# Optimization experiments

Hardware: AMD Instinct MI355X
Metric: run time of the kernel (lower is better)

Reference implementation:

```python
import jax, jax.numpy as jnp
import numpy as np

B, S, F = 4, 2048, 8
D, H, L, FF = 256, 8, 2, 1024
DH = D // H
NSK, NPAT = 2000, 64
DQ = D // 4  # pattern/feat sub-embedding width


def setup_inputs() -> dict:
    key = jax.random.key(0)
    ks = jax.random.split(key, 32)
    r = lambda i, shape: jax.random.normal(ks[i], shape, jnp.float32) * 0.02
    return {
        'interactions': jax.random.randint(ks[0], (B, S), 0, 2 * NSK),
        'patterns': jax.random.randint(ks[1], (B, S), 0, NPAT),
        'forget_features': jax.random.normal(ks[2], (B, S, F), jnp.float32),
        'inter_emb': r(3, (2 * NSK, D)),
        'pattern_emb': r(4, (NPAT, DQ)),
        'feat_W': r(5, (F, DQ)), 'feat_b': jnp.zeros((DQ,), jnp.float32),
        'in_W': r(6, (D + 2 * DQ, D)), 'in_b': jnp.zeros((D,), jnp.float32),
        'time_W': r(7, (1, D)), 'time_b': jnp.zeros((D,), jnp.float32),
        'pos_W': r(8, (1, D)), 'pos_b': jnp.zeros((D,), jnp.float32),
        'Wq': r(9, (L, D, H, DH)), 'bq': jnp.zeros((L, H, DH), jnp.float32),
        'Wk': r(10, (L, D, H, DH)), 'bk': jnp.zeros((L, H, DH), jnp.float32),
        'Wv': r(11, (L, D, H, DH)), 'bv': jnp.zeros((L, H, DH), jnp.float32),
        'Wo': r(12, (L, H, DH, D)), 'bo': jnp.zeros((L, D), jnp.float32),
        'kerple_p': jnp.full((L, H, 1, 1), 0.5, jnp.float32),
        'kerple_a': jnp.zeros((L, H, 1, 1), jnp.float32),
        'ln1_g': jnp.ones((L, D), jnp.float32), 'ln1_b': jnp.zeros((L, D), jnp.float32),
        'ln2_g': jnp.ones((L, D), jnp.float32), 'ln2_b': jnp.zeros((L, D), jnp.float32),
        'ffn_W1': r(13, (L, D, FF)), 'ffn_b1': jnp.zeros((L, FF), jnp.float32),
        'ffn_W2': r(14, (L, FF, D)), 'ffn_b2': jnp.zeros((L, D), jnp.float32),
        'out_W': r(15, (D, NSK)), 'out_b': jnp.zeros((NSK,), jnp.float32),
    }


def _ln(x, g, b, eps=1e-6):
    m = jnp.mean(x, -1, keepdims=True)
    v = jnp.mean(jnp.square(x - m), -1, keepdims=True)
    return g * (x - m) * jax.lax.rsqrt(v + eps) + b


def reference(interactions, patterns, forget_features, inter_emb, pattern_emb,
              feat_W, feat_b, in_W, in_b, time_W, time_b, pos_W, pos_b,
              Wq, bq, Wk, bk, Wv, bv, Wo, bo, kerple_p, kerple_a,
              ln1_g, ln1_b, ln2_g, ln2_b, ffn_W1, ffn_b1, ffn_W2, ffn_b2,
              out_W, out_b):
    inter_e = inter_emb[interactions]                      # [B,S,D]
    pat_e = pattern_emb[patterns]                          # [B,S,D/4]
    feat_e = forget_features @ feat_W + feat_b             # [B,S,D/4]
    x = jnp.concatenate([inter_e, pat_e, feat_e], -1) @ in_W + in_b  # [B,S,D]
    elapsed = forget_features[:, :, 0:1]
    time_enc = jnp.tanh(elapsed @ time_W + time_b)
    pos = jnp.arange(S, dtype=jnp.float32)[None, :, None] / jnp.float32(S)
    pos_enc = pos @ pos_W + pos_b
    x = x + time_enc + pos_enc

    positions = jnp.arange(S, dtype=jnp.float32)
    dist = jnp.maximum(positions[:, None] - positions[None, :], 0.0)  # [S,S]
    causal_bias = jnp.triu(jnp.full((S, S), -1e9, jnp.float32), 1)    # [S,S]
    inv_sqrt_dh = 1.0 / jnp.sqrt(jnp.float32(DH))

    for i in range(L):
        p = jax.nn.softplus(kerple_p[i])                   # [H,1,1]
        a = jax.nn.softplus(kerple_a[i])
        bias = causal_bias[None] - p * jnp.log1p(a * dist[None])  # [H,S,S]
        q = jnp.einsum('bsd,dhk->bshk', x, Wq[i]) + bq[i]
        k = jnp.einsum('bsd,dhk->bshk', x, Wk[i]) + bk[i]
        v = jnp.einsum('bsd,dhk->bshk', x, Wv[i]) + bv[i]
        scores = jnp.einsum('bshk,bthk->bhst', q, k) * inv_sqrt_dh + bias[None]
        attn = jax.nn.softmax(scores, axis=-1)
        o = jnp.einsum('bhst,bthk->bshk', attn, v)
        attn_out = jnp.einsum('bshk,hkd->bsd', o, Wo[i]) + bo[i]
        x = _ln(x + attn_out, ln1_g[i], ln1_b[i])
        h = jax.nn.gelu(x @ ffn_W1[i] + ffn_b1[i], approximate=False)
        ffn_out = h @ ffn_W2[i] + ffn_b2[i]
        x = _ln(x + ffn_out, ln2_g[i], ln2_b[i])
    return x @ out_W + out_b
```

## Files before the change

### kernel.cpp

```cpp
#include <hip/hip_runtime.h>
#include <math.h>

#define SEQ   2048
#define BATCH 4
#define NTOK  8192
#define DM    256
#define NHD   8
#define DHD   32
#define DFF   1024
#define NSKC  2000

typedef __attribute__((ext_vector_type(8))) short short8;
typedef __attribute__((ext_vector_type(4))) float f32x4;
typedef unsigned short ushort_t;

#define QPRE ((float)(0.17677669529663687 * 1.4426950408889634))

#define SPERM(i) (((i) & ~31) | (((i) & 15) << 1) | (((i) >> 4) & 1))

__device__ __forceinline__ ushort_t f2bf(float x) {
    union { float f; unsigned u; } c; c.f = x;
    unsigned r = c.u + 0x7FFFu + ((c.u >> 16) & 1u);
    return (ushort_t)(r >> 16);
}

#if __has_builtin(__builtin_amdgcn_cvt_pk_bf16_f32)
typedef __attribute__((ext_vector_type(2))) __bf16 bf16x2_t;
__device__ __forceinline__ unsigned pack_bf16(float a, float b) {
    bf16x2_t r = __builtin_amdgcn_cvt_pk_bf16_f32(a, b);
    union { bf16x2_t v; unsigned u; } c; c.v = r;
    return c.u;
}
#else
__device__ __forceinline__ unsigned pack_bf16(float a, float b) {
    return (unsigned)f2bf(a) | ((unsigned)f2bf(b) << 16);
}
#endif

__device__ __forceinline__ float bf2f(ushort_t x) {
    union { unsigned u; float f; } c; c.u = ((unsigned)x) << 16;
    return c.f;
}

struct ConvSeg { const float* src; ushort_t* dst; int K; int N; int ntx; int base; int kperm; };
struct ConvArgs { ConvSeg s[14]; };

__global__ __launch_bounds__(256) void convert_kernel(ConvArgs args) {
    int bid = blockIdx.x;
    int si = 0;
#pragma unroll
    for (int i = 1; i < 14; i++) if (bid >= args.s[i].base) si = i;
    ConvSeg sg = args.s[si];
    int local = bid - sg.base;
    int ty = local / sg.ntx;
    int tx = local - ty * sg.ntx;
    int n0 = tx * 32, k0 = ty * 32;
    __shared__ float T[32][33];
    int tid = threadIdx.x;
    int tn = tid & 31, tk4 = tid >> 5;
#pragma unroll
    for (int i = 0; i < 4; i++) {
        int kl = tk4 + i * 8;
        float v = 0.0f;
        if (n0 + tn < sg.N) v = sg.src[(size_t)(k0 + kl) * sg.N + n0 + tn];
        T[kl][tn] = v;
    }
    __syncthreads();
    int tk = tid & 31, tn4 = tid >> 5;
    int tks = sg.kperm ? (((tk & 15) << 1) | ((tk >> 4) & 1)) : tk;
#pragma unroll
    for (int i = 0; i < 4; i++) {
        int nl = tn4 + i * 8;
        sg.dst[(size_t)(n0 + nl) * sg.K + k0 + tks] = f2bf(T[tk][nl]);
    }
}

__global__ __launch_bounds__(384) void concat_kernel(
    const int* __restrict__ interactions, const int* __restrict__ patterns,
    const float* __restrict__ ff, const float* __restrict__ inter_emb,
    const float* __restrict__ pattern_emb, const float* __restrict__ feat_W,
    const float* __restrict__ feat_b, ushort_t* __restrict__ out)
{
    int tok = blockIdx.x;
    int j = threadIdx.x;
    float v;
    if (j < 256) {
        v = inter_emb[(size_t)interactions[tok] * 256 + j];
    } else if (j < 320) {
        v = pattern_emb[patterns[tok] * 64 + (j - 256)];
    } else {
        int c = j - 320;
        float acc = feat_b[c];
#pragma unroll
        for (int f = 0; f < 8; f++) acc += ff[tok * 8 + f] * feat_W[f * 64 + c];
        v = acc;
    }
    out[(size_t)tok * 384 + j] = f2bf(v);
}

__global__ __launch_bounds__(256) void ln_kernel(
    float* __restrict__ x, const ushort_t* __restrict__ r,
    const float* __restrict__ g, const float* __restrict__ b,
    ushort_t* __restrict__ xb)
{
    int tok = blockIdx.x;
    int d = threadIdx.x;
    int ds = SPERM(d);
    size_t row = (size_t)tok * DM;
    float v = x[row + d] + bf2f(r[row + ds]);
    float s1 = v, s2 = v * v;
#pragma unroll
    for (int off = 32; off > 0; off >>= 1) {
        s1 += __shfl_down(s1, off, 64);
        s2 += __shfl_down(s2, off, 64);
    }
    __shared__ float red1[4], red2[4];
    int wid = d >> 6, lane = d & 63;
    if (lane == 0) { red1[wid] = s1; red2[wid] = s2; }
    __syncthreads();
    s1 = red1[0] + red1[1] + red1[2] + red1[3];
    s2 = red2[0] + red2[1] + red2[2] + red2[3];
    float mean = s1 * (1.0f / 256.0f);
    float var = s2 * (1.0f / 256.0f) - mean * mean;
    float inv = rsqrtf(var + 1e-6f);
    float nv = g[d] * (v - mean) * inv + b[d];
    x[row + d] = nv;
    xb[row + ds] = f2bf(nv);
}

__global__ __launch_bounds__(256) void gemm64(
    const ushort_t* __restrict__ A, const ushort_t* __restrict__ Bt,
    int M, int N, int K, int mode,
    float* __restrict__ Cf, ushort_t* __restrict__ Cb,
    const float* __restrict__ b0,
    const float* __restrict__ ffg, const float* __restrict__ tW,
    const float* __restrict__ tb, const float* __restrict__ pW,
    const float* __restrict__ pb)
{
    __shared__ ushort_t As[2][64][40];
    __shared__ ushort_t Bs[2][64][40];
    int m0 = blockIdx.x * 64, n0 = blockIdx.y * 64;
    int tid = threadIdx.x;
    int wv = tid >> 6, lane = tid & 63;
    int quad = lane >> 4, l16 = lane & 15;
    int srow = tid >> 2, sc = (tid & 3) << 3;

    f32x4 acc[4];
#pragma unroll
    for (int j = 0; j < 4; j++) acc[j] = (f32x4){0.f, 0.f, 0.f, 0.f};

    uint4 pa = *(const uint4*)&A[(size_t)(m0 + srow) * K + sc];
    uint4 pbv = *(const uint4*)&Bt[(size_t)(n0 + srow) * K + sc];
    *(uint4*)&As[0][srow][sc] = pa;
    *(uint4*)&Bs[0][srow][sc] = pbv;

    int mrow = wv * 16;
    for (int k0 = 0; k0 < K; k0 += 32) {
        int cur = (k0 >> 5) & 1;
        __syncthreads();
        bool more = (k0 + 32 < K);
        if (more) {
            pa = *(const uint4*)&A[(size_t)(m0 + srow) * K + k0 + 32 + sc];
            pbv = *(const uint4*)&Bt[(size_t)(n0 + srow) * K + k0 + 32 + sc];
        }
        short8 af = *(const short8*)&As[cur][mrow + l16][quad * 8];
        short8 bf0 = *(const short8*)&Bs[cur][l16][quad * 8];
        short8 bf1 = *(const short8*)&Bs[cur][16 + l16][quad * 8];
        short8 bf2 = *(const short8*)&Bs[cur][32 + l16][quad * 8];
        short8 bf3 = *(const short8*)&Bs[cur][48 + l16][quad * 8];
        acc[0] = __builtin_amdgcn_mfma_f32_16x16x32_bf16(af, bf0, acc[0], 0, 0, 0);
        acc[1] = __builtin_amdgcn_mfma_f32_16x16x32_bf16(af, bf1, acc[1], 0, 0, 0);
        acc[2] = __builtin_amdgcn_mfma_f32_16x16x32_bf16(af, bf2, acc[2], 0, 0, 0);
        acc[3] = __builtin_amdgcn_mfma_f32_16x16x32_bf16(af, bf3, acc[3], 0, 0, 0);
        if (more) {
            *(uint4*)&As[cur ^ 1][srow][sc] = pa;
            *(uint4*)&Bs[cur ^ 1][srow][sc] = pbv;
        }
    }

#pragma unroll
    for (int r = 0; r < 4; r++) {
        int m = m0 + mrow + quad * 4 + r;
        if (mode == 4) {
            int s = m & (SEQ - 1);
            float el = ffg[m * 8];
            float pos = (float)s * (1.0f / (float)SEQ);
#pragma unroll
            for (int nt = 0; nt < 4; nt += 2) {
                int nlo = n0 + nt * 16 + l16;
                int nhi = nlo + 16;
                float v0 = acc[nt][r] + b0[nlo] + tanhf(el * tW[nlo] + tb[nlo]) + pos * pW[nlo] + pb[nlo];
                float v1 = acc[nt + 1][r] + b0[nhi] + tanhf(el * tW[nhi] + tb[nhi]) + pos * pW[nhi] + pb[nhi];
                Cf[(size_t)m * N + nlo] = v0;
                Cf[(size_t)m * N + nhi] = v1;
                *(unsigned*)&Cb[(size_t)m * N + n0 + nt * 16 + 2 * l16] = pack_bf16(v0, v1);
            }
        } else {
#pragma unroll
            for (int nt = 0; nt < 4; nt += 2) {
                int nlo = n0 + nt * 16 + l16;
                float v0 = acc[nt][r] + b0[nlo];
                float v1 = acc[nt + 1][r] + b0[nlo + 16];
                *(unsigned*)&Cb[(size_t)m * N + n0 + nt * 16 + 2 * l16] = pack_bf16(v0, v1);
            }
        }
    }
}

__global__ __launch_bounds__(256) void gemm_db(
    const ushort_t* __restrict__ A, const ushort_t* __restrict__ Bt,
    int M, int N, int K, int mode,
    ushort_t* __restrict__ Cb, ushort_t* __restrict__ Ck, ushort_t* __restrict__ Cv,
    const float* __restrict__ b0, const float* __restrict__ b1,
    const float* __restrict__ b2)
{
    __shared__ ushort_t As[2][128][40];
    __shared__ ushort_t Bs[2][64][40];
    int m0 = blockIdx.x * 128, n0 = blockIdx.y * 64;
    int tid = threadIdx.x;
    int wv = tid >> 6, lane = tid & 63;
    int quad = lane >> 4, l16 = lane & 15;
    int srow = tid >> 2, sc = (tid & 3) << 3;

    f32x4 acc[2][4];
#pragma unroll
    for (int i = 0; i < 2; i++)
#pragma unroll
        for (int j = 0; j < 4; j++) acc[i][j] = (f32x4){0.f, 0.f, 0.f, 0.f};

    uint4 pa0 = *(const uint4*)&A[(size_t)(m0 + srow) * K + sc];
    uint4 pa1 = *(const uint4*)&A[(size_t)(m0 + 64 + srow) * K + sc];
    uint4 pbb = *(const uint4*)&Bt[(size_t)(n0 + srow) * K + sc];
    *(uint4*)&As[0][srow][sc] = pa0;
    *(uint4*)&As[0][64 + srow][sc] = pa1;
    *(uint4*)&Bs[0][srow][sc] = pbb;

    int msub = wv * 32;
    for (int k0 = 0; k0 < K; k0 += 32) {
        int cur = (k0 >> 5) & 1;
        __syncthreads();
        bool more = (k0 + 32 < K);
        if (more) {
            pa0 = *(const uint4*)&A[(size_t)(m0 + srow) * K + k0 + 32 + sc];
            pa1 = *(const uint4*)&A[(size_t)(m0 + 64 + srow) * K + k0 + 32 + sc];
            pbb = *(const uint4*)&Bt[(size_t)(n0 + srow) * K + k0 + 32 + sc];
        }
        short8 af0 = *(const short8*)&As[cur][msub + l16][quad * 8];
        short8 af1 = *(const short8*)&As[cur][msub + 16 + l16][quad * 8];
        short8 bf0 = *(const short8*)&Bs[cur][l16][quad * 8];
        short8 bf1 = *(const short8*)&Bs[cur][16 + l16][quad * 8];
        short8 bf2 = *(const short8*)&Bs[cur][32 + l16][quad * 8];
        short8 bf3 = *(const short8*)&Bs[cur][48 + l16][quad * 8];
        acc[0][0] = __builtin_amdgcn_mfma_f32_16x16x32_bf16(af0, bf0, acc[0][0], 0, 0, 0);
        acc[0][1] = __builtin_amdgcn_mfma_f32_16x16x32_bf16(af0, bf1, acc[0][1], 0, 0, 0);
        acc[0][2] = __builtin_amdgcn_mfma_f32_16x16x32_bf16(af0, bf2, acc[0][2], 0, 0, 0);
        acc[0][3] = __builtin_amdgcn_mfma_f32_16x16x32_bf16(af0, bf3, acc[0][3], 0, 0, 0);
        acc[1][0] = __builtin_amdgcn_mfma_f32_16x16x32_bf16(af1, bf0, acc[1][0], 0, 0, 0);
        acc[1][1] = __builtin_amdgcn_mfma_f32_16x16x32_bf16(af1, bf1, acc[1][1], 0, 0, 0);
        acc[1][2] = __builtin_amdgcn_mfma_f32_16x16x32_bf16(af1, bf2, acc[1][2], 0, 0, 0);
        acc[1][3] = __builtin_amdgcn_mfma_f32_16x16x32_bf16(af1, bf3, acc[1][3], 0, 0, 0);
        if (more) {
            *(uint4*)&As[cur ^ 1][srow][sc] = pa0;
            *(uint4*)&As[cur ^ 1][64 + srow][sc] = pa1;
            *(uint4*)&Bs[cur ^ 1][srow][sc] = pbb;
        }
    }

#pragma unroll
    for (int mt = 0; mt < 2; mt++) {
#pragma unroll
        for (int nt = 0; nt < 4; nt += 2) {
            int nlo = n0 + nt * 16 + l16;
#pragma unroll
            for (int r = 0; r < 4; r++) {
                int m = m0 + msub + mt * 16 + quad * 4 + r;
                float vlo = acc[mt][nt][r];
                float vhi = acc[mt][nt + 1][r];
                if (mode == 1) {
                    float t0 = vlo + b0[nlo];
                    float t1 = vhi + b0[nlo + 16];
                    t0 = 0.5f * t0 * (1.0f + erff(t0 * 0.70710678118654752f));
                    t1 = 0.5f * t1 * (1.0f + erff(t1 * 0.70710678118654752f));
                    *(unsigned*)&Cb[(size_t)m * N + n0 + nt * 16 + 2 * l16] = pack_bf16(t0, t1);
                } else {
                    int which = nlo >> 8, idx = nlo & 255;
                    int hh = idx >> 5;
                    int s = m & (SEQ - 1), b = m >> 11;
                    if (which == 0) {
                        float q0 = (vlo + b0[idx]) * QPRE;
                        float q1 = (vhi + b0[idx + 16]) * QPRE;
                        *(unsigned*)&Cb[(((size_t)(b * NHD + hh)) * SEQ + s) * DHD + 2 * l16] = pack_bf16(q0, q1);
                    } else if (which == 1) {
                        float k0v = vlo + b1[idx];
                        float k1v = vhi + b1[idx + 16];
                        *(unsigned*)&Ck[(((size_t)(b * NHD + hh)) * SEQ + s) * DHD + 2 * l16] = pack_bf16(k0v, k1v);
                    } else {
                        int sp = (s & ~31) | (((s & 15) << 1) | ((s >> 4) & 1));
                        Cv[(((size_t)(b * NHD + hh)) * DHD + l16) * SEQ + sp] = f2bf(vlo + b2[idx]);
                        Cv[(((size_t)(b * NHD + hh)) * DHD + l16 + 16) * SEQ + sp] = f2bf(vhi + b2[idx + 16]);
                    }
                }
            }
        }
    }
}

__global__ __launch_bounds__(256) void gemm_out(
    const ushort_t* __restrict__ A, const ushort_t* __restrict__ Bt,
    int M, int N, int K,
    float* __restrict__ Cf, const float* __restrict__ b0, int Nreal)
{
    __shared__ ushort_t As[2][128][40];
    __shared__ ushort_t Bs[2][128][40];
    int m0 = blockIdx.x * 128, n0 = blockIdx.y * 128;
    int tid = threadIdx.x;
    int wv = tid >> 6, lane = tid & 63;
    int quad = lane >> 4, l16 = lane & 15;
    int wm = (wv >> 1) * 64, wn = (wv & 1) * 64;
    int srow = tid >> 1, sc = (tid & 1) << 4;

    f32x4 acc[4][4];
#pragma unroll
    for (int i = 0; i < 4; i++)
#pragma unroll
        for (int j = 0; j < 4; j++) acc[i][j] = (f32x4){0.f, 0.f, 0.f, 0.f};

    uint4 pa0 = *(const uint4*)&A[(size_t)(m0 + srow) * K + sc];
    uint4 pa1 = *(const uint4*)&A[(size_t)(m0 + srow) * K + sc + 8];
    uint4 pb0 = *(const uint4*)&Bt[(size_t)(n0 + srow) * K + sc];
    uint4 pb1 = *(const uint4*)&Bt[(size_t)(n0 + srow) * K + sc + 8];
    *(uint4*)&As[0][srow][sc] = pa0;
    *(uint4*)&As[0][srow][sc + 8] = pa1;
    *(uint4*)&Bs[0][srow][sc] = pb0;
    *(uint4*)&Bs[0][srow][sc + 8] = pb1;

    for (int k0 = 0; k0 < K; k0 += 32) {
        int cur = (k0 >> 5) & 1;
        __syncthreads();
        bool more = (k0 + 32 < K);
        if (more) {
            pa0 = *(const uint4*)&A[(size_t)(m0 + srow) * K + k0 + 32 + sc];
            pa1 = *(const uint4*)&A[(size_t)(m0 + srow) * K + k0 + 32 + sc + 8];
            pb0 = *(const uint4*)&Bt[(size_t)(n0 + srow) * K + k0 + 32 + sc];
            pb1 = *(const uint4*)&Bt[(size_t)(n0 + srow) * K + k0 + 32 + sc + 8];
        }
        short8 af[4], bf[4];
#pragma unroll
        for (int i = 0; i < 4; i++) {
            af[i] = *(const short8*)&As[cur][wm + i * 16 + l16][quad * 8];
            bf[i] = *(const short8*)&Bs[cur][wn + i * 16 + l16][quad * 8];
        }
#pragma unroll
        for (int i = 0; i < 4; i++)
#pragma unroll
            for (int j = 0; j < 4; j++)
                acc[i][j] = __builtin_amdgcn_mfma_f32_16x16x32_bf16(af[i], bf[j], acc[i][j], 0, 0, 0);
        if (more) {
            *(uint4*)&As[cur ^ 1][srow][sc] = pa0;
            *(uint4*)&As[cur ^ 1][srow][sc + 8] = pa1;
            *(uint4*)&Bs[cur ^ 1][srow][sc] = pb0;
            *(uint4*)&Bs[cur ^ 1][srow][sc + 8] = pb1;
        }
    }

#pragma unroll
    for (int i = 0; i < 4; i++) {
#pragma unroll
        for (int j = 0; j < 4; j++) {
            int n = n0 + wn + j * 16 + l16;
            if (n < Nreal) {
#pragma unroll
                for (int r = 0; r < 4; r++) {
                    int m = m0 + wm + i * 16 + quad * 4 + r;
                    Cf[(size_t)m * Nreal + n] = acc[i][j][r] + b0[n];
                }
            }
        }
    }
}

__global__ __launch_bounds__(256) void attn_mfma(
    const ushort_t* __restrict__ qb, const ushort_t* __restrict__ kb,
    const ushort_t* __restrict__ vtb, const float* __restrict__ kp,
    const float* __restrict__ ka, ushort_t* __restrict__ ob)
{
    int h = blockIdx.y, b = blockIdx.z;
    int tid = threadIdx.x, wv = tid >> 6, lane = tid & 63;
    int quad = lane >> 4, l16 = lane & 15;
    int pair = wv >> 1, parity = wv & 1;

    __shared__ float tabs[2112];
    __shared__ ushort_t P2[4][2][16 * 40];
    __shared__ float Cmb[2][64][28];

    float p = log1pf(__expf(kp[h]));
    float a = log1pf(__expf(ka[h]));
    for (int i = tid; i < 2112; i += 256) {
        float w = 0.0f;
        if (i >= 64) w = exp2f(-p * __log2f(fmaf(a, (float)(i - 64), 1.0f)));
        tabs[i] = w;
    }
    __syncthreads();

    int bh = b * NHD + h;
    const ushort_t* Qh = qb + (size_t)bh * SEQ * DHD;
    const ushort_t* Kh = kb + (size_t)bh * SEQ * DHD;
    const ushort_t* Vh = vtb + (size_t)bh * DHD * SEQ;

    int pj = blockIdx.x * 2 + pair;
    int tlo = pj, thi = 127 - pj;
    int qlo0 = tlo * 16, qhi0 = thi * 16;

    short8 qfl = *(const short8*)&Qh[(qlo0 + l16) * DHD + quad * 8];
    short8 qfh = *(const short8*)&Qh[(qhi0 + l16) * DHD + quad * 8];
    f32x4 ol0 = (f32x4){0.f,0.f,0.f,0.f}, ol1 = (f32x4){0.f,0.f,0.f,0.f};
    f32x4 oh0 = (f32x4){0.f,0.f,0.f,0.f}, oh1 = (f32x4){0.f,0.f,0.f,0.f};
    float lsl[4] = {0.f,0.f,0.f,0.f}, lsh[4] = {0.f,0.f,0.f,0.f};
    ushort_t* Pl = &P2[wv][0][0];
    ushort_t* Ph = &P2[wv][1][0];

    int nch_hi = (thi + 2) >> 1;
    int nch_lo = (tlo + 2) >> 1;
    int qsrh = qhi0 + quad * 4;
    int qsrl = qlo0 + quad * 4;

    for (int ch = parity; ch < nch_hi; ch += 2) {
        int k0 = ch * 32;
        short8 kf0 = *(const short8*)&Kh[(k0 + l16) * DHD + quad * 8];
        short8 kf1 = *(const short8*)&Kh[(k0 + 16 + l16) * DHD + quad * 8];
        short8 vf0 = *(const short8*)&Vh[l16 * SEQ + k0 + quad * 8];
        short8 vf1 = *(const short8*)&Vh[(16 + l16) * SEQ + k0 + quad * 8];
        f32x4 z = (f32x4){0.f,0.f,0.f,0.f};

        f32x4 s0 = __builtin_amdgcn_mfma_f32_16x16x32_bf16(qfh, kf0, z, 0, 0, 0);
        f32x4 s1 = __builtin_amdgcn_mfma_f32_16x16x32_bf16(qfh, kf1, z, 0, 0, 0);
        {
            const float* tp = &tabs[qsrh - k0 - l16 + 48];
#pragma unroll
            for (int r = 0; r < 4; r++) {
                float e0 = exp2f(s0[r]) * tp[16 + r];
                float e1 = exp2f(s1[r]) * tp[r];
                lsh[r] += e0 + e1;
                *(unsigned*)&Ph[(quad * 4 + r) * 40 + l16 * 2] = pack_bf16(e0, e1);
            }
        }
        bool do_lo = (ch < nch_lo);
        if (do_lo) {
            f32x4 t0 = __builtin_amdgcn_mfma_f32_16x16x32_bf16(qfl, kf0, z, 0, 0, 0);
            f32x4 t1 = __builtin_amdgcn_mfma_f32_16x16x32_bf16(qfl, kf1, z, 0, 0, 0);
            const float* tq = &tabs[qsrl - k0 - l16 + 48];
#pragma unroll
            for (int r = 0; r < 4; r++) {
                float e0 = exp2f(t0[r]) * tq[16 + r];
                float e1 = exp2f(t1[r]) * tq[r];
                lsl[r] += e0 + e1;
                *(unsigned*)&Pl[(quad * 4 + r) * 40 + l16 * 2] = pack_bf16(e0, e1);
            }
        }

        __builtin_amdgcn_wave_barrier();
        short8 pfh = *(const short8*)&Ph[l16 * 40 + quad * 8];
        oh0 = __builtin_amdgcn_mfma_f32_16x16x32_bf16(pfh, vf0, oh0, 0, 0, 0);
        oh1 = __builtin_amdgcn_mfma_f32_16x16x32_bf16(pfh, vf1, oh1, 0, 0, 0);
        if (do_lo) {
            short8 pfl = *(const short8*)&Pl[l16 * 40 + quad * 8];
            ol0 = __builtin_amdgcn_mfma_f32_16x16x32_bf16(pfl, vf0, ol0, 0, 0, 0);
            ol1 = __builtin_amdgcn_mfma_f32_16x16x32_bf16(pfl, vf1, ol1, 0, 0, 0);
        }
    }

    if (parity == 1) {
        float* cp = &Cmb[pair][lane][0];
        *(float4*)&cp[0]  = (float4){oh0[0], oh0[1], oh0[2], oh0[3]};
        *(float4*)&cp[4]  = (float4){oh1[0], oh1[1], oh1[2], oh1[3]};
        *(float4*)&cp[8]  = (float4){ol0[0], ol0[1], ol0[2], ol0[3]};
        *(float4*)&cp[12] = (float4){ol1[0], ol1[1], ol1[2], ol1[3]};
        *(float4*)&cp[16] = (float4){lsh[0], lsh[1], lsh[2], lsh[3]};
        *(float4*)&cp[20] = (float4){lsl[0], lsl[1], lsl[2], lsl[3]};
    }
    __syncthreads();
    if (parity == 0) {
        const float* cp = &Cmb[pair][lane][0];
#pragma unroll
        for (int i = 0; i < 4; i++) {
            oh0[i] += cp[i];      oh1[i] += cp[4 + i];
            ol0[i] += cp[8 + i];  ol1[i] += cp[12 + i];
            lsh[i] += cp[16 + i]; lsl[i] += cp[20 + i];
        }
#pragma unroll
        for (int r = 0; r < 4; r++) {
#pragma unroll
            for (int off = 1; off < 16; off <<= 1) {
                lsh[r] += __shfl_xor(lsh[r], off, 16);
                lsl[r] += __shfl_xor(lsl[r], off, 16);
            }
        }
#pragma unroll
        for (int r = 0; r < 4; r++) {
            float rh = 1.0f / lsh[r];
            float rl = 1.0f / lsl[r];
            size_t bh_ = ((size_t)(b * SEQ + qsrh + r)) * DM + h * DHD;
            size_t bl_ = ((size_t)(b * SEQ + qsrl + r)) * DM + h * DHD;
            *(unsigned*)&ob[bh_ + 2 * l16] = pack_bf16(oh0[r] * rh, oh1[r] * rh);
            *(unsigned*)&ob[bl_ + 2 * l16] = pack_bf16(ol0[r] * rl, ol1[r] * rl);
        }
    }
}

extern "C" void kernel_launch(void* const* d_in, const int* in_sizes, int n_in,
                              void* d_out, int out_size, void* d_ws, size_t ws_size,
                              hipStream_t stream) {
    const int*   interactions = (const int*)d_in[0];
    const int*   patterns     = (const int*)d_in[1];
    const float* ff           = (const float*)d_in[2];
    const float* inter_emb    = (const float*)d_in[3];
    const float* pattern_emb  = (const float*)d_in[4];
    const float* feat_W       = (const float*)d_in[5];
    const float* feat_b       = (const float*)d_in[6];
    const float* in_W         = (const float*)d_in[7];
    const float* in_b         = (const float*)d_in[8];
    const float* time_W       = (const float*)d_in[9];
    const float* time_b       = (const float*)d_in[10];
    const float* pos_W        = (const float*)d_in[11];
    const float* pos_b        = (const float*)d_in[12];
    const float* Wq           = (const float*)d_in[13];
    const float* bq           = (const float*)d_in[14];
    const float* Wk           = (const float*)d_in[15];
    const float* bk           = (const float*)d_in[16];
    const float* Wv           = (const float*)d_in[17];
    const float* bv           = (const float*)d_in[18];
    const float* Wo           = (const float*)d_in[19];
    const float* bo           = (const float*)d_in[20];
    const float* kerple_p     = (const float*)d_in[21];
    const float* kerple_a     = (const float*)d_in[22];
    const float* ln1_g        = (const float*)d_in[23];
    const float* ln1_b        = (const float*)d_in[24];
    const float* ln2_g        = (const float*)d_in[25];
    const float* ln2_b        = (const float*)d_in[26];
    const float* ffn_W1       = (const float*)d_in[27];
    const float* ffn_b1       = (const float*)d_in[28];
    const float* ffn_W2       = (const float*)d_in[29];
    const float* ffn_b2       = (const float*)d_in[30];
    const float* out_W        = (const float*)d_in[31];
    const float* out_b        = (const float*)d_in[32];
    float* out = (float*)d_out;

    char* wsb = (char*)d_ws;
    const size_t MB = 1024 * 1024;
    float*    x    = (float*)(wsb + 0);
    ushort_t* tmpb = (ushort_t*)(wsb + 8  * MB);
    ushort_t* xb   = (ushort_t*)(wsb + 16 * MB);
    ushort_t* qbuf = (ushort_t*)(wsb + 20 * MB);
    ushort_t* kbuf = (ushort_t*)(wsb + 24 * MB);
    ushort_t* vtbf = (ushort_t*)(wsb + 28 * MB);
    ushort_t* shrd = (ushort_t*)(wsb + 32 * MB);
    ushort_t* cbuf = shrd;
    ushort_t* o_bf = shrd;
    ushort_t* h_bf = shrd;
    char* wp = wsb + 48 * MB;
    ushort_t* inWt  = (ushort_t*)wp;  wp += 256  * 384 * 2;
    ushort_t* qkvWt = (ushort_t*)wp;  wp += 2 * 768 * 256 * 2;
    ushort_t* WoT   = (ushort_t*)wp;  wp += 2 * 256 * 256 * 2;
    ushort_t* W1T   = (ushort_t*)wp;  wp += 2 * 1024 * 256 * 2;
    ushort_t* W2T   = (ushort_t*)wp;  wp += 2 * 256 * 1024 * 2;
    ushort_t* outWt = (ushort_t*)wp;  wp += 2048 * 256 * 2;

    ConvArgs ca;
    int D2 = 256 * 256;
    int base = 0, ib = 0;
    auto addseg = [&](const float* src, ushort_t* dst, int K, int N, int Npad, int kp) {
        ca.s[ib].src = src; ca.s[ib].dst = dst; ca.s[ib].K = K; ca.s[ib].N = N;
        ca.s[ib].ntx = Npad / 32; ca.s[ib].base = base; ca.s[ib].kperm = kp;
        base += (Npad / 32) * (K / 32); ib++;
    };
    addseg(in_W,            inWt,           384,  256,  256,  0);
    addseg(Wq,              qkvWt,          256,  256,  256,  1);
    addseg(Wk,              qkvWt + 1 * D2, 256,  256,  256,  1);
    addseg(Wv,              qkvWt + 2 * D2, 256,  256,  256,  1);
    addseg(Wq + D2,         qkvWt + 3 * D2, 256,  256,  256,  1);
    addseg(Wk + D2,         qkvWt + 4 * D2, 256,  256,  256,  1);
    addseg(Wv + D2,         qkvWt + 5 * D2, 256,  256,  256,  1);
    addseg(Wo,              WoT,            256,  256,  256,  1);
    addseg(Wo + D2,         WoT + D2,       256,  256,  256,  1);
    addseg(ffn_W1,          W1T,            256,  1024, 1024, 1);
    addseg(ffn_W1 + 4 * D2, W1T + 4 * D2,   256,  1024, 1024, 1);
    addseg(ffn_W2,          W2T,            1024, 256,  256,  1);
    addseg(ffn_W2 + 4 * D2, W2T + 4 * D2,   1024, 256,  256,  1);
    addseg(out_W,           outWt,          256,  2000, 2048, 1);
    convert_kernel<<<base, 256, 0, stream>>>(ca);

    concat_kernel<<<NTOK, 384, 0, stream>>>(interactions, patterns, ff,
                                            inter_emb, pattern_emb, feat_W, feat_b, cbuf);
    gemm64<<<dim3(128, 4), 256, 0, stream>>>(cbuf, inWt, NTOK, 256, 384, 4,
                                             x, xb, in_b, ff, time_W, time_b, pos_W, pos_b);

    for (int l = 0; l < 2; l++) {
        gemm_db<<<dim3(64, 12), 256, 0, stream>>>(
            xb, qkvWt + (size_t)l * 768 * 256, NTOK, 768, 256, 2,
            qbuf, kbuf, vtbf, bq + l * 256, bk + l * 256, bv + l * 256);
        attn_mfma<<<dim3(32, NHD, BATCH), 256, 0, stream>>>(
            qbuf, kbuf, vtbf, kerple_p + l * NHD, kerple_a + l * NHD, o_bf);
        gemm64<<<dim3(128, 4), 256, 0, stream>>>(
            o_bf, WoT + (size_t)l * D2, NTOK, 256, 256, 5,
            nullptr, tmpb, bo + l * 256, nullptr, nullptr, nullptr, nullptr, nullptr);
        ln_kernel<<<NTOK, 256, 0, stream>>>(x, tmpb, ln1_g + l * 256, ln1_b + l * 256, xb);
        gemm_db<<<dim3(64, 16), 256, 0, stream>>>(
            xb, W1T + (size_t)l * 4 * D2, NTOK, 1024, 256, 1,
            h_bf, nullptr, nullptr, ffn_b1 + l * 1024, nullptr, nullptr);
        gemm64<<<dim3(128, 4), 256, 0, stream>>>(
            h_bf, W2T + (size_t)l * 4 * D2, NTOK, 256, 1024, 5,
            nullptr, tmpb, ffn_b2 + l * 256, nullptr, nullptr, nullptr, nullptr, nullptr);
        ln_kernel<<<NTOK, 256, 0, stream>>>(x, tmpb, ln2_g + l * 256, ln2_b + l * 256, xb);
    }

    gemm_out<<<dim3(64, 16), 256, 0, stream>>>(
        xb, outWt, NTOK, 2048, 256, out, out_b, NSKC);
}
```

Baseline: 418.5 us.

## Split attention key chunks across four waves per query-tile pair with K prefetch

Each attention block now handles one lo/hi query-tile pair, and its four waves stride over key chunks by four instead of two waves per pair striding by two. The grid doubles to 64 blocks in x. Partial outputs and row sums are combined through a two-stage shared-memory tree reduction, and the P scratch buffer is aliased onto the combine buffer to cut LDS use. Next-iteration K fragments are prefetched into registers to hide load latency. The cost is extra __syncthreads and reduction work per block, plus possible load imbalance for short low tiles.

```diff
diff --git a/kernel.cpp b/kernel.cpp
--- a/kernel.cpp
+++ b/kernel.cpp
@@ -387,11 +387,10 @@
     int h = blockIdx.y, b = blockIdx.z;
     int tid = threadIdx.x, wv = tid >> 6, lane = tid & 63;
     int quad = lane >> 4, l16 = lane & 15;
-    int pair = wv >> 1, parity = wv & 1;
 
     __shared__ float tabs[2112];
-    __shared__ ushort_t P2[4][2][16 * 40];
-    __shared__ float Cmb[2][64][28];
+    __shared__ __align__(16) float Cmbf[2][64][28];
+    ushort_t* P2 = (ushort_t*)&Cmbf[0][0][0];
 
     float p = log1pf(__expf(kp[h]));
     float a = log1pf(__expf(ka[h]));
@@ -407,7 +406,7 @@
     const ushort_t* Kh = kb + (size_t)bh * SEQ * DHD;
     const ushort_t* Vh = vtb + (size_t)bh * DHD * SEQ;
 
-    int pj = blockIdx.x * 2 + pair;
+    int pj = blockIdx.x;
     int tlo = pj, thi = 127 - pj;
     int qlo0 = tlo * 16, qhi0 = thi * 16;
 
@@ -416,20 +415,33 @@
     f32x4 ol0 = (f32x4){0.f,0.f,0.f,0.f}, ol1 = (f32x4){0.f,0.f,0.f,0.f};
     f32x4 oh0 = (f32x4){0.f,0.f,0.f,0.f}, oh1 = (f32x4){0.f,0.f,0.f,0.f};
     float lsl[4] = {0.f,0.f,0.f,0.f}, lsh[4] = {0.f,0.f,0.f,0.f};
-    ushort_t* Pl = &P2[wv][0][0];
-    ushort_t* Ph = &P2[wv][1][0];
+    ushort_t* Pl = P2 + wv * 1280;
+    ushort_t* Ph = Pl + 640;
 
     int nch_hi = (thi + 2) >> 1;
     int nch_lo = (tlo + 2) >> 1;
     int qsrh = qhi0 + quad * 4;
     int qsrl = qlo0 + quad * 4;
 
-    for (int ch = parity; ch < nch_hi; ch += 2) {
+    int ch = wv;
+    short8 kf0n, kf1n;
+    {
         int k0 = ch * 32;
-        short8 kf0 = *(const short8*)&Kh[(k0 + l16) * DHD + quad * 8];
-        short8 kf1 = *(const short8*)&Kh[(k0 + 16 + l16) * DHD + quad * 8];
+        kf0n = *(const short8*)&Kh[(k0 + l16) * DHD + quad * 8];
+        kf1n = *(const short8*)&Kh[(k0 + 16 + l16) * DHD + quad * 8];
+    }
+
+    for (; ch < nch_hi; ch += 4) {
+        int k0 = ch * 32;
+        short8 kf0 = kf0n, kf1 = kf1n;
         short8 vf0 = *(const short8*)&Vh[l16 * SEQ + k0 + quad * 8];
         short8 vf1 = *(const short8*)&Vh[(16 + l16) * SEQ + k0 + quad * 8];
+        int chn = ch + 4;
+        if (chn < nch_hi) {
+            int kn = chn * 32;
+            kf0n = *(const short8*)&Kh[(kn + l16) * DHD + quad * 8];
+            kf1n = *(const short8*)&Kh[(kn + 16 + l16) * DHD + quad * 8];
+        }
         f32x4 z = (f32x4){0.f,0.f,0.f,0.f};
 
         f32x4 s0 = __builtin_amdgcn_mfma_f32_16x16x32_bf16(qfh, kf0, z, 0, 0, 0);
@@ -469,8 +481,9 @@
         }
     }
 
-    if (parity == 1) {
-        float* cp = &Cmb[pair][lane][0];
+    __syncthreads();
+    float* cp = &Cmbf[wv >> 1][lane][0];
+    if (wv & 1) {
         *(float4*)&cp[0]  = (float4){oh0[0], oh0[1], oh0[2], oh0[3]};
         *(float4*)&cp[4]  = (float4){oh1[0], oh1[1], oh1[2], oh1[3]};
         *(float4*)&cp[8]  = (float4){ol0[0], ol0[1], ol0[2], ol0[3]};
@@ -479,13 +492,32 @@
         *(float4*)&cp[20] = (float4){lsl[0], lsl[1], lsl[2], lsl[3]};
     }
     __syncthreads();
-    if (parity == 0) {
-        const float* cp = &Cmb[pair][lane][0];
+    if (!(wv & 1)) {
 #pragma unroll
         for (int i = 0; i < 4; i++) {
             oh0[i] += cp[i];      oh1[i] += cp[4 + i];
             ol0[i] += cp[8 + i];  ol1[i] += cp[12 + i];
             lsh[i] += cp[16 + i]; lsl[i] += cp[20 + i];
+        }
+    }
+    __syncthreads();
+    if (wv == 2) {
+        float* c0 = &Cmbf[0][lane][0];
+        *(float4*)&c0[0]  = (float4){oh0[0], oh0[1], oh0[2], oh0[3]};
+        *(float4*)&c0[4]  = (float4){oh1[0], oh1[1], oh1[2], oh1[3]};
+        *(float4*)&c0[8]  = (float4){ol0[0], ol0[1], ol0[2], ol0[3]};
+        *(float4*)&c0[12] = (float4){ol1[0], ol1[1], ol1[2], ol1[3]};
+        *(float4*)&c0[16] = (float4){lsh[0], lsh[1], lsh[2], lsh[3]};
+        *(float4*)&c0[20] = (float4){lsl[0], lsl[1], lsl[2], lsl[3]};
+    }
+    __syncthreads();
+    if (wv == 0) {
+        const float* c0 = &Cmbf[0][lane][0];
+#pragma unroll
+        for (int i = 0; i < 4; i++) {
+            oh0[i] += c0[i];      oh1[i] += c0[4 + i];
+            ol0[i] += c0[8 + i];  ol1[i] += c0[12 + i];
+            lsh[i] += c0[16 + i]; lsl[i] += c0[20 + i];
         }
 #pragma unroll
         for (int r = 0; r < 4; r++) {
@@ -598,7 +630,7 @@
         gemm_db<<<dim3(64, 12), 256, 0, stream>>>(
             xb, qkvWt + (size_t)l * 768 * 256, NTOK, 768, 256, 2,
             qbuf, kbuf, vtbf, bq + l * 256, bk + l * 256, bv + l * 256);
-        attn_mfma<<<dim3(32, NHD, BATCH), 256, 0, stream>>>(
+        attn_mfma<<<dim3(64, NHD, BATCH), 256, 0, stream>>>(
             qbuf, kbuf, vtbf, kerple_p + l * NHD, kerple_a + l * NHD, o_bf);
         gemm64<<<dim3(128, 4), 256, 0, stream>>>(
             o_bf, WoT + (size_t)l * D2, NTOK, 256, 256, 5,
```

Result: no change. 416.2 us (-0.6%).
